# Kernel optimization log

Hardware: AMD Instinct MI355X
Metric: run time of the kernel (lower is better)

## Reference

```python
import jax, jax.numpy as jnp
import numpy as np

INPUT_SIZE = 1024
HIDDEN_SIZE = 1024
W_RANK = 64
U_RANK = 64
BATCH = 32768


def setup_inputs() -> dict:
    key = jax.random.key(0)
    ks = jax.random.split(key, 16)
    p = lambda k, shape: 0.1 * jax.random.normal(k, shape, dtype=jnp.float32)
    return {
        "x": jax.random.normal(ks[0], (BATCH, INPUT_SIZE), dtype=jnp.float32),
        "h": jax.random.normal(ks[1], (BATCH, HIDDEN_SIZE), dtype=jnp.float32),
        "W": p(ks[2], (INPUT_SIZE, W_RANK)),
        "W1": p(ks[3], (W_RANK, HIDDEN_SIZE)),
        "W2": p(ks[4], (W_RANK, HIDDEN_SIZE)),
        "W3": p(ks[5], (W_RANK, HIDDEN_SIZE)),
        "U": p(ks[6], (HIDDEN_SIZE, U_RANK)),
        "U1": p(ks[7], (U_RANK, HIDDEN_SIZE)),
        "U2": p(ks[8], (U_RANK, HIDDEN_SIZE)),
        "U3": p(ks[9], (U_RANK, HIDDEN_SIZE)),
        "U1_diag": p(ks[10], (HIDDEN_SIZE,)),
        "U2_diag": p(ks[11], (HIDDEN_SIZE,)),
        "U3_diag": p(ks[12], (HIDDEN_SIZE,)),
        "bias_r": jnp.ones((1, HIDDEN_SIZE), dtype=jnp.float32),
        "bias_gate": jnp.ones((1, HIDDEN_SIZE), dtype=jnp.float32),
        "bias_update": jnp.ones((1, HIDDEN_SIZE), dtype=jnp.float32),
    }


def reference(x, h, W, W1, W2, W3, U, U1, U2, U3,
              U1_diag, U2_diag, U3_diag, bias_r, bias_gate, bias_update):
    # Low-rank projections shared across gates (matches torch matmul order)
    xW = x @ W          # [B, wRank]
    hU = h @ U          # [B, uRank]
    wVal1 = xW @ W1
    wVal2 = xW @ W2
    wVal3 = xW @ W3
    uVal1 = hU @ U1
    uVal2 = hU @ U2
    r = jax.nn.sigmoid(wVal1 + uVal1 + h * U1_diag + bias_r)
    z = jax.nn.sigmoid(wVal2 + uVal2 + h * U2_diag + bias_gate)
    rh = r * h
    matVal_c = wVal3 + (rh @ U) @ U3 + rh * U3_diag
    c_tilda = jnp.tanh(matVal_c + bias_update)
    h_next = z * h + (1.0 - z) * c_tilda
    return h_next
```

## Files before the change

### kernel.cpp

```cpp
#include <hip/hip_runtime.h>
#include <hip/hip_bf16.h>


typedef __attribute__((ext_vector_type(8))) short short8;
typedef __attribute__((ext_vector_type(4))) float f32x4;
typedef __attribute__((ext_vector_type(4))) float f4;

#define WS_UT   65536
#define WS_P1T  131072
#define WS_P2T  262144
#define WS_P3T  393216
#define WS_A12  524288
#define WS_RHU  4718592

__device__ __forceinline__ short f2bf(float f) {
  unsigned u = __builtin_bit_cast(unsigned, f);
  u += 0x7FFFu + ((u >> 16) & 1u);
  return (short)(u >> 16);
}
__device__ __forceinline__ short8 cvt8(f4 a, f4 b) {
  short8 r;
#pragma unroll
  for (int j = 0; j < 4; ++j) { r[j] = f2bf(a[j]); r[4 + j] = f2bf(b[j]); }
  return r;
}
__device__ __forceinline__ f32x4 mfma16(short8 a, short8 b, f32x4 c) {
  return __builtin_amdgcn_mfma_f32_16x16x32_bf16(a, b, c, 0, 0, 0);
}
__device__ __forceinline__ short8 ldg8(const short* p) {
  return *reinterpret_cast<const short8*>(p);
}
__device__ __forceinline__ f4 ldf4(const float* p) {
  return *reinterpret_cast<const f4*>(p);
}

__device__ __forceinline__ void cp16(void* l, const void* g) {
  __builtin_amdgcn_global_load_lds(
      (const __attribute__((address_space(1))) void*)g,
      (__attribute__((address_space(3))) void*)l, 16, 0, 0);
}
#define VWAIT(N) do { asm volatile("s_waitcnt vmcnt(" #N ")" ::: "memory"); \
                      __builtin_amdgcn_sched_barrier(0); } while (0)

__device__ __forceinline__ short8 rd128s(const short* b, int row, int col) {
  return *reinterpret_cast<const short8*>(b + row * 128 + (col ^ ((row & 7) << 3)));
}
__device__ __forceinline__ void wr128s(short* b, int row, int col8, short8 v) {
  *reinterpret_cast<short8*>(b + row * 128 + (col8 ^ ((row & 7) << 3))) = v;
}
__device__ __forceinline__ void wr64(short* b, int row, int col, short v) {
  b[row * 64 + (col ^ ((row & 7) << 3))] = v;
}
__device__ __forceinline__ short8 rd64(const short* b, int row, int col) {
  return *reinterpret_cast<const short8*>(b + row * 64 + (col ^ ((row & 7) << 3)));
}

#define LOG2E 1.4426950408889634f
__device__ __forceinline__ float sigm_f(float v) {
  return __builtin_amdgcn_rcpf(1.f + __builtin_amdgcn_exp2f(-v * LOG2E));
}
__device__ __forceinline__ float tanh_f(float v) {
  float t = __builtin_amdgcn_exp2f(v * (2.f * LOG2E));
  return 1.f - 2.f * __builtin_amdgcn_rcpf(t + 1.f);
}

__global__ void prep_kernel(const float* __restrict__ W,  const float* __restrict__ W1,
                            const float* __restrict__ W2, const float* __restrict__ W3,
                            const float* __restrict__ U,  const float* __restrict__ U1,
                            const float* __restrict__ U2, const float* __restrict__ U3,
                            short* __restrict__ ws) {
  int i = blockIdx.x * blockDim.x + threadIdx.x;
  float v;
  if (i < 65536) {
    int n = i >> 10, k = i & 1023;
    v = W[k * 64 + n];
  } else if (i < 131072) {
    int j = i - 65536;
    int n = j >> 10, k = j & 1023;
    v = U[k * 64 + n];
  } else {
    int j = i - 131072;
    int sel = j >> 17;
    int jj = j & 131071;
    int n = jj >> 7, k = jj & 127;
    const float* Wk = sel == 0 ? W1 : sel == 1 ? W2 : W3;
    const float* Uk = sel == 0 ? U1 : sel == 1 ? U2 : U3;
    v = (k < 64) ? Wk[k * 1024 + n] : Uk[(k - 64) * 1024 + n];
  }
  ws[i] = f2bf(v);
}

__global__ __launch_bounds__(256, 4) void k1_a12(
    const float* __restrict__ x, const float* __restrict__ h,
    const short* __restrict__ ws, short* __restrict__ A12) {
  __shared__ __align__(16) float sS[2][4][16 * 64];

  const int tid = threadIdx.x;
  const int w = tid >> 6, l = tid & 63, l15 = l & 15, lg = l >> 4;
  const int m = w >> 1, half = w & 1;
  const int sr = blockIdx.x * 32 + half * 16;
  const float* src = m ? h : x;
  const short* Bt  = ws + m * WS_UT;

  const int srow = l >> 4;
  const int slin = (l & 15) * 16;

  auto STAGE = [&](int c, int b) {
#pragma unroll
    for (int i = 0; i < 4; ++i) {
      int r = i * 4 + srow;
      int kb = slin ^ ((r & 7) << 4);
      cp16((char*)&sS[b][w][0] + i * 1024,
           (const char*)(src + (size_t)(sr + r) * 1024 + c * 64) + kb);
    }
  };
  auto WLOAD = [&](int c, short8* bw) {
#pragma unroll
    for (int ks = 0; ks < 2; ++ks)
#pragma unroll
      for (int cf = 0; cf < 4; ++cf)
        bw[ks * 4 + cf] =
            ldg8(Bt + (size_t)(cf * 16 + l15) * 1024 + c * 64 + ks * 32 + lg * 8);
  };

  f32x4 acc[4] = {};
  short8 bwb[2][8];
  STAGE(0, 0);
  WLOAD(0, bwb[0]);
#pragma unroll
  for (int c = 0; c < 16; ++c) {
    if (c < 15) {
      WLOAD(c + 1, bwb[(c + 1) & 1]);
      STAGE(c + 1, (c + 1) & 1);
      VWAIT(12);
    } else {
      VWAIT(0);
    }
    const char* Bb = (const char*)&sS[c & 1][w][0];
    const int s = (l15 & 7) << 4;
    const short8* bw = bwb[c & 1];
#pragma unroll
    for (int ks = 0; ks < 2; ++ks) {
      const int kb0 = (ks * 32 + lg * 8) * 4;
      f4 pa = *(const f4*)(Bb + l15 * 256 + (kb0 ^ s));
      f4 pb = *(const f4*)(Bb + l15 * 256 + ((kb0 + 16) ^ s));
      short8 av = cvt8(pa, pb);
#pragma unroll
      for (int cf = 0; cf < 4; ++cf) acc[cf] = mfma16(av, bw[ks * 4 + cf], acc[cf]);
    }
  }
#pragma unroll
  for (int cf = 0; cf < 4; ++cf)
#pragma unroll
    for (int j = 0; j < 4; ++j)
      A12[(size_t)(sr + lg * 4 + j) * 128 + m * 64 + cf * 16 + l15] = f2bf(acc[cf][j]);
}

__global__ __launch_bounds__(256, 2) void k23_rhu(
    const float* __restrict__ h, const float* __restrict__ u1d,
    const float* __restrict__ biasR,
    const short* __restrict__ ws, const short* __restrict__ A12,
    short* __restrict__ rhU) {
  const short* Ut  = ws + WS_UT;
  const short* P1t = ws + WS_P1T;
  __shared__ __align__(16) float hS[2][4][16 * 64];
  __shared__ __align__(16) short sT[4][16 * 64];

  const int tid = threadIdx.x;
  const int w = tid >> 6, l = tid & 63, l15 = l & 15, lg = l >> 4;
  const int sr = blockIdx.x * 64 + w * 16;

  const int srow = l >> 4;
  const int slin = (l & 15) * 16;

  auto STAGE = [&](int t, int b) {
#pragma unroll
    for (int i = 0; i < 4; ++i) {
      int r = i * 4 + srow;
      int kb = slin ^ ((r & 7) << 4);
      cp16((char*)&hS[b][w][0] + i * 1024,
           (const char*)(h + (size_t)(sr + r) * 1024 + t * 64) + kb);
    }
  };

  short8 a12[4];
#pragma unroll
  for (int k0 = 0; k0 < 4; ++k0)
    a12[k0] = ldg8(A12 + (size_t)(sr + l15) * 128 + k0 * 32 + lg * 8);

  f32x4 accU[4] = {};
  STAGE(0, 0);
#pragma unroll 1
  for (int tt = 0; tt < 16; ++tt) {
    const int n0 = tt * 64;
    short8 b1[4][4], bu[2][4];
    float d1_[4], br_[4];
#pragma unroll
    for (int ks = 0; ks < 4; ++ks)
#pragma unroll
      for (int cf = 0; cf < 4; ++cf)
        b1[ks][cf] = ldg8(P1t + (size_t)(n0 + cf * 16 + l15) * 128 + ks * 32 + lg * 8);
#pragma unroll
    for (int kk = 0; kk < 2; ++kk)
#pragma unroll
      for (int cf = 0; cf < 4; ++cf)
        bu[kk][cf] = ldg8(Ut + (size_t)(cf * 16 + l15) * 1024 + n0 + kk * 32 + lg * 8);
#pragma unroll
    for (int cf = 0; cf < 4; ++cf) {
      d1_[cf] = u1d[n0 + cf * 16 + l15];
      br_[cf] = biasR[n0 + cf * 16 + l15];
    }
    if (tt < 15) { STAGE(tt + 1, (tt + 1) & 1); VWAIT(4); }
    else         { VWAIT(0); }
    const char* H = (const char*)&hS[tt & 1][w][0];

    float hv[4][4];
#pragma unroll
    for (int cf = 0; cf < 4; ++cf)
#pragma unroll
      for (int j = 0; j < 4; ++j) {
        int rr = lg * 4 + j;
        hv[cf][j] = *(const float*)(H + rr * 256 + ((cf * 64 + l15 * 4) ^ ((rr & 7) << 4)));
      }
    f32x4 accR[4] = {};
#pragma unroll
    for (int ks = 0; ks < 4; ++ks)
#pragma unroll
      for (int cf = 0; cf < 4; ++cf) accR[cf] = mfma16(a12[ks], b1[ks][cf], accR[cf]);
#pragma unroll
    for (int cf = 0; cf < 4; ++cf)
#pragma unroll
      for (int j = 0; j < 4; ++j) {
        float rv = sigm_f(accR[cf][j] + hv[cf][j] * d1_[cf] + br_[cf]);
        wr64(&sT[w][0], lg * 4 + j, cf * 16 + l15, f2bf(rv * hv[cf][j]));
      }
    short8 arh0 = rd64(&sT[w][0], l15, lg * 8);
    short8 arh1 = rd64(&sT[w][0], l15, 32 + lg * 8);
#pragma unroll
    for (int cf = 0; cf < 4; ++cf) accU[cf] = mfma16(arh0, bu[0][cf], accU[cf]);
#pragma unroll
    for (int cf = 0; cf < 4; ++cf) accU[cf] = mfma16(arh1, bu[1][cf], accU[cf]);
  }
#pragma unroll
  for (int cf = 0; cf < 4; ++cf)
#pragma unroll
    for (int j = 0; j < 4; ++j)
      rhU[(size_t)(sr + lg * 4 + j) * 64 + cf * 16 + l15] = f2bf(accU[cf][j]);
}

__global__ __launch_bounds__(256, 2) void k4_out(
    const float* __restrict__ h,
    const float* __restrict__ u1d, const float* __restrict__ u2d,
    const float* __restrict__ u3d,
    const float* __restrict__ biasR, const float* __restrict__ biasZ,
    const float* __restrict__ biasU,
    const short* __restrict__ ws, const short* __restrict__ A12,
    const short* __restrict__ rhU, float* __restrict__ out) {
  __shared__ __align__(16) short sB1[64 * 128], sB2[64 * 128], sB3[64 * 128];
  __shared__ __align__(16) float hS[2][4][16 * 64];

  const int tid = threadIdx.x;
  const int w = tid >> 6, l = tid & 63, l15 = l & 15, lg = l >> 4;
  const int ct = blockIdx.x & 15, rc = blockIdx.x >> 4;
  const int n0 = ct * 64;

#pragma unroll
  for (int mat = 0; mat < 3; ++mat) {
    const short* srcw = (mat == 0) ? (ws + WS_P1T) : (mat == 1) ? (ws + WS_P2T) : (ws + WS_P3T);
    short* dst = (mat == 0) ? sB1 : (mat == 1) ? sB2 : sB3;
#pragma unroll
    for (int i = 0; i < 4; ++i) {
      int id = tid + i * 256;
      int row = id >> 4, gc = id & 15;
      wr128s(dst, row, gc * 8, ldg8(srcw + (size_t)(n0 + row) * 128 + gc * 8));
    }
  }
  float d1_[4], d2_[4], d3_[4], br_[4], bz_[4], bu_[4];
#pragma unroll
  for (int cf = 0; cf < 4; ++cf) {
    const int cc = n0 + cf * 16 + l15;
    d1_[cf] = u1d[cc]; d2_[cf] = u2d[cc]; d3_[cf] = u3d[cc];
    br_[cf] = biasR[cc]; bz_[cf] = biasZ[cc]; bu_[cf] = biasU[cc];
  }
  __syncthreads();

  const int srow = l >> 4;
  const int slin = (l & 15) * 16;
  auto STAGE = [&](int rnd, int b) {
    const int sb = rc * 512 + rnd * 64 + w * 16;
#pragma unroll
    for (int i = 0; i < 4; ++i) {
      int r = i * 4 + srow;
      int kb = slin ^ ((r & 7) << 4);
      cp16((char*)&hS[b][w][0] + i * 1024,
           (const char*)(h + (size_t)(sb + r) * 1024 + n0) + kb);
    }
  };

  STAGE(0, 0);
#pragma unroll 1
  for (int rnd = 0; rnd < 8; ++rnd) {
    const int sr = rc * 512 + rnd * 64 + w * 16;
    short8 a12[4], arhu[2];
#pragma unroll
    for (int k0 = 0; k0 < 4; ++k0)
      a12[k0] = ldg8(A12 + (size_t)(sr + l15) * 128 + k0 * 32 + lg * 8);
#pragma unroll
    for (int kk = 0; kk < 2; ++kk)
      arhu[kk] = ldg8(rhU + (size_t)(sr + l15) * 64 + kk * 32 + lg * 8);
    if (rnd < 7) { STAGE(rnd + 1, (rnd + 1) & 1); VWAIT(4); }
    else         { VWAIT(0); }
    const char* H = (const char*)&hS[rnd & 1][w][0];

    float hv[4][4];
#pragma unroll
    for (int cf = 0; cf < 4; ++cf)
#pragma unroll
      for (int j = 0; j < 4; ++j) {
        int rr = lg * 4 + j;
        hv[cf][j] = *(const float*)(H + rr * 256 + ((cf * 64 + l15 * 4) ^ ((rr & 7) << 4)));
      }

    f32x4 aR[4] = {}, aZ[4] = {}, aC[4] = {};
#pragma unroll
    for (int k0 = 0; k0 < 4; ++k0) {
      const short8 a3 = (k0 < 2) ? a12[k0] : arhu[k0 - 2];
#pragma unroll
      for (int cf = 0; cf < 4; ++cf) {
        aR[cf] = mfma16(a12[k0], rd128s(sB1, cf * 16 + l15, k0 * 32 + lg * 8), aR[cf]);
        aZ[cf] = mfma16(a12[k0], rd128s(sB2, cf * 16 + l15, k0 * 32 + lg * 8), aZ[cf]);
        aC[cf] = mfma16(a3,      rd128s(sB3, cf * 16 + l15, k0 * 32 + lg * 8), aC[cf]);
      }
    }
#pragma unroll
    for (int cf = 0; cf < 4; ++cf) {
      const int cc = n0 + cf * 16 + l15;
#pragma unroll
      for (int j = 0; j < 4; ++j) {
        const size_t gi = (size_t)(sr + lg * 4 + j) * 1024 + cc;
        const float hvj = hv[cf][j];
        float rv = sigm_f(aR[cf][j] + hvj * d1_[cf] + br_[cf]);
        float zv = sigm_f(aZ[cf][j] + hvj * d2_[cf] + bz_[cf]);
        float cv = tanh_f(aC[cf][j] + rv * hvj * d3_[cf] + bu_[cf]);
        out[gi] = zv * hvj + (1.f - zv) * cv;
      }
    }
  }
}

extern "C" void kernel_launch(void* const* d_in, const int* in_sizes, int n_in,
                              void* d_out, int out_size, void* d_ws, size_t ws_size,
                              hipStream_t stream) {
  const float* x   = (const float*)d_in[0];
  const float* h   = (const float*)d_in[1];
  const float* W   = (const float*)d_in[2];
  const float* W1  = (const float*)d_in[3];
  const float* W2  = (const float*)d_in[4];
  const float* W3  = (const float*)d_in[5];
  const float* U   = (const float*)d_in[6];
  const float* U1  = (const float*)d_in[7];
  const float* U2  = (const float*)d_in[8];
  const float* U3  = (const float*)d_in[9];
  const float* u1d = (const float*)d_in[10];
  const float* u2d = (const float*)d_in[11];
  const float* u3d = (const float*)d_in[12];
  const float* bR  = (const float*)d_in[13];
  const float* bZ  = (const float*)d_in[14];
  const float* bU  = (const float*)d_in[15];
  short* ws  = (short*)d_ws;
  short* A12 = ws + WS_A12;
  short* rhU = ws + WS_RHU;

  prep_kernel<<<2048, 256, 0, stream>>>(W, W1, W2, W3, U, U1, U2, U3, ws);
  k1_a12<<<1024, 256, 0, stream>>>(x, h, ws, A12);
  k23_rhu<<<512, 256, 0, stream>>>(h, u1d, bR, ws, A12, rhU);
  k4_out<<<1024, 256, 0, stream>>>(h, u1d, u2d, u3d, bR, bZ, bU, ws, A12, rhU, (float*)d_out);
}
```

Before: 244.8 us.

## Split k23 hidden dimension across wave pairs with LDS reduction, drop async h staging

The rhU kernel now assigns each 16-row strip to two waves, each covering half of the 1024 hidden columns, and sums their partial rhU accumulators through shared memory before writing. The async double-buffered staging of h into LDS is removed in favour of direct global loads, and the weight loads are inlined into the MFMA calls. Grid size doubles and launch bounds rise to 4 blocks per CU to raise occupancy and parallelism. In exchange it adds a block-wide sync, an LDS reduction, and uncoalesced-looking direct h loads that lose the explicit prefetch overlap.

```diff
diff --git a/kernel.cpp b/kernel.cpp
--- a/kernel.cpp
+++ b/kernel.cpp
@@ -156,32 +156,21 @@
       A12[(size_t)(sr + lg * 4 + j) * 128 + m * 64 + cf * 16 + l15] = f2bf(acc[cf][j]);
 }
 
-__global__ __launch_bounds__(256, 2) void k23_rhu(
+__global__ __launch_bounds__(256, 4) void k23_rhu(
     const float* __restrict__ h, const float* __restrict__ u1d,
     const float* __restrict__ biasR,
     const short* __restrict__ ws, const short* __restrict__ A12,
     short* __restrict__ rhU) {
   const short* Ut  = ws + WS_UT;
   const short* P1t = ws + WS_P1T;
-  __shared__ __align__(16) float hS[2][4][16 * 64];
-  __shared__ __align__(16) short sT[4][16 * 64];
+  __shared__ __align__(16) short sT[4][2][16 * 64];
+  __shared__ __align__(16) float sRed[2][2][16 * 64];
 
   const int tid = threadIdx.x;
-  const int w = tid >> 6, l = tid & 63, l15 = l & 15, lg = l >> 4;
-  const int sr = blockIdx.x * 64 + w * 16;
-
-  const int srow = l >> 4;
-  const int slin = (l & 15) * 16;
-
-  auto STAGE = [&](int t, int b) {
-#pragma unroll
-    for (int i = 0; i < 4; ++i) {
-      int r = i * 4 + srow;
-      int kb = slin ^ ((r & 7) << 4);
-      cp16((char*)&hS[b][w][0] + i * 1024,
-           (const char*)(h + (size_t)(sr + r) * 1024 + t * 64) + kb);
-    }
-  };
+  const int w   = tid >> 6, l = tid & 63, l15 = l & 15, lg = l >> 4;
+  const int s   = w >> 1;
+  const int ch  = w & 1;
+  const int sr  = blockIdx.x * 32 + s * 16;
 
   short8 a12[4];
 #pragma unroll
@@ -189,63 +178,72 @@
     a12[k0] = ldg8(A12 + (size_t)(sr + l15) * 128 + k0 * 32 + lg * 8);
 
   f32x4 accU[4] = {};
-  STAGE(0, 0);
 #pragma unroll 1
-  for (int tt = 0; tt < 16; ++tt) {
-    const int n0 = tt * 64;
-    short8 b1[4][4], bu[2][4];
-    float d1_[4], br_[4];
-#pragma unroll
-    for (int ks = 0; ks < 4; ++ks)
+  for (int tt = 0; tt < 8; ++tt) {
+    const int n0 = ch * 512 + tt * 64;
+
+    float hv[4][4];
+#pragma unroll
+    for (int cf = 0; cf < 4; ++cf)
+#pragma unroll
+      for (int j = 0; j < 4; ++j)
+        hv[cf][j] = h[(size_t)(sr + lg * 4 + j) * 1024 + n0 + cf * 16 + l15];
+
+    f32x4 accR[4] = {};
+#pragma unroll
+    for (int k0 = 0; k0 < 4; ++k0)
 #pragma unroll
       for (int cf = 0; cf < 4; ++cf)
-        b1[ks][cf] = ldg8(P1t + (size_t)(n0 + cf * 16 + l15) * 128 + ks * 32 + lg * 8);
-#pragma unroll
-    for (int kk = 0; kk < 2; ++kk)
-#pragma unroll
-      for (int cf = 0; cf < 4; ++cf)
-        bu[kk][cf] = ldg8(Ut + (size_t)(cf * 16 + l15) * 1024 + n0 + kk * 32 + lg * 8);
+        accR[cf] = mfma16(a12[k0],
+            ldg8(P1t + (size_t)(n0 + cf * 16 + l15) * 128 + k0 * 32 + lg * 8),
+            accR[cf]);
+
+    short* sw = &sT[w][tt & 1][0];
 #pragma unroll
     for (int cf = 0; cf < 4; ++cf) {
-      d1_[cf] = u1d[n0 + cf * 16 + l15];
-      br_[cf] = biasR[n0 + cf * 16 + l15];
-    }
-    if (tt < 15) { STAGE(tt + 1, (tt + 1) & 1); VWAIT(4); }
-    else         { VWAIT(0); }
-    const char* H = (const char*)&hS[tt & 1][w][0];
-
-    float hv[4][4];
-#pragma unroll
-    for (int cf = 0; cf < 4; ++cf)
-#pragma unroll
-      for (int j = 0; j < 4; ++j) {
-        int rr = lg * 4 + j;
-        hv[cf][j] = *(const float*)(H + rr * 256 + ((cf * 64 + l15 * 4) ^ ((rr & 7) << 4)));
-      }
-    f32x4 accR[4] = {};
-#pragma unroll
-    for (int ks = 0; ks < 4; ++ks)
-#pragma unroll
-      for (int cf = 0; cf < 4; ++cf) accR[cf] = mfma16(a12[ks], b1[ks][cf], accR[cf]);
-#pragma unroll
-    for (int cf = 0; cf < 4; ++cf)
-#pragma unroll
-      for (int j = 0; j < 4; ++j) {
-        float rv = sigm_f(accR[cf][j] + hv[cf][j] * d1_[cf] + br_[cf]);
-        wr64(&sT[w][0], lg * 4 + j, cf * 16 + l15, f2bf(rv * hv[cf][j]));
-      }
-    short8 arh0 = rd64(&sT[w][0], l15, lg * 8);
-    short8 arh1 = rd64(&sT[w][0], l15, 32 + lg * 8);
-#pragma unroll
-    for (int cf = 0; cf < 4; ++cf) accU[cf] = mfma16(arh0, bu[0][cf], accU[cf]);
-#pragma unroll
-    for (int cf = 0; cf < 4; ++cf) accU[cf] = mfma16(arh1, bu[1][cf], accU[cf]);
-  }
-#pragma unroll
-  for (int cf = 0; cf < 4; ++cf)
-#pragma unroll
-    for (int j = 0; j < 4; ++j)
-      rhU[(size_t)(sr + lg * 4 + j) * 64 + cf * 16 + l15] = f2bf(accU[cf][j]);
+      const int cc = n0 + cf * 16 + l15;
+      const float d1 = u1d[cc], b_r = biasR[cc];
+#pragma unroll
+      for (int j = 0; j < 4; ++j) {
+        float rv = sigm_f(accR[cf][j] + hv[cf][j] * d1 + b_r);
+        wr64(sw, lg * 4 + j, cf * 16 + l15, f2bf(rv * hv[cf][j]));
+      }
+    }
+    short8 arh0 = rd64(sw, l15, lg * 8);
+    short8 arh1 = rd64(sw, l15, 32 + lg * 8);
+#pragma unroll
+    for (int cf = 0; cf < 4; ++cf)
+      accU[cf] = mfma16(arh0,
+          ldg8(Ut + (size_t)(cf * 16 + l15) * 1024 + n0 + lg * 8), accU[cf]);
+#pragma unroll
+    for (int cf = 0; cf < 4; ++cf)
+      accU[cf] = mfma16(arh1,
+          ldg8(Ut + (size_t)(cf * 16 + l15) * 1024 + n0 + 32 + lg * 8), accU[cf]);
+  }
+
+  {
+    float* fT = &sRed[s][ch][0];
+#pragma unroll
+    for (int cf = 0; cf < 4; ++cf)
+#pragma unroll
+      for (int j = 0; j < 4; ++j) {
+        int row = lg * 4 + j, col = cf * 16 + l15;
+        fT[row * 64 + (col ^ ((row & 7) << 2))] = accU[cf][j];
+      }
+  }
+  __syncthreads();
+  if (ch == 0) {
+    const float* f0 = &sRed[s][0][0];
+    const float* f1 = &sRed[s][1][0];
+#pragma unroll
+    for (int cf = 0; cf < 4; ++cf)
+#pragma unroll
+      for (int j = 0; j < 4; ++j) {
+        int row = lg * 4 + j, col = cf * 16 + l15;
+        int idx = row * 64 + (col ^ ((row & 7) << 2));
+        rhU[(size_t)(sr + row) * 64 + col] = f2bf(f0[idx] + f1[idx]);
+      }
+  }
 }
 
 __global__ __launch_bounds__(256, 2) void k4_out(
@@ -373,6 +371,6 @@
 
   prep_kernel<<<2048, 256, 0, stream>>>(W, W1, W2, W3, U, U1, U2, U3, ws);
   k1_a12<<<1024, 256, 0, stream>>>(x, h, ws, A12);
-  k23_rhu<<<512, 256, 0, stream>>>(h, u1d, bR, ws, A12, rhU);
+  k23_rhu<<<1024, 256, 0, stream>>>(h, u1d, bR, ws, A12, rhU);
   k4_out<<<1024, 256, 0, stream>>>(h, u1d, u2d, u3d, bR, bZ, bU, ws, A12, rhU, (float*)d_out);
 }
```

Result: no change. 240.7 us (median of 2 runs) (-1.7%).
